# Kernel tuning notes

Hardware: AMD Instinct MI355X
Metric: run time of the kernel (lower is better)

Reference implementation:

```python
import jax, jax.numpy as jnp
import numpy as np

N_NODES = 20000
N_EDGES = 640000
HIDDEN = 256
MSG = 64  # discrete message of MSG binary symbols -> 2*MSG one-hot bits
TAU = 0.5


def setup_inputs() -> dict:
    key = jax.random.key(0)
    ks = jax.random.split(key, 12)
    x = jax.random.normal(ks[0], (N_NODES, HIDDEN), dtype=jnp.float32)
    h = jax.random.normal(ks[1], (N_NODES, HIDDEN), dtype=jnp.float32)
    src = jax.random.randint(ks[2], (N_EDGES,), 0, N_NODES)
    dst = jax.random.randint(ks[3], (N_EDGES,), 0, N_NODES)
    u = jax.random.uniform(ks[4], (N_EDGES, MSG, 2), dtype=jnp.float32,
                           minval=1e-6, maxval=1.0 - 1e-6)
    gumbel = -jnp.log(-jnp.log(u))  # standard Gumbel noise
    def lin(k, out_f, in_f):
        bound = 1.0 / np.sqrt(in_f)
        kw, kb = jax.random.split(k)
        W = jax.random.uniform(kw, (out_f, in_f), jnp.float32, -bound, bound)
        b = jax.random.uniform(kb, (out_f,), jnp.float32, -bound, bound)
        return W, b
    W_enc, b_enc = lin(ks[5], 2 * MSG, 2 * HIDDEN)          # f_enc
    W_dec, b_dec = lin(ks[6], 2 * MSG, 2 * MSG)             # f_dec
    W_ih, b_ih = lin(ks[7], 3 * HIDDEN, HIDDEN + 2 * MSG)   # GRUCell input weights
    W_hh, b_hh = lin(ks[8], 3 * HIDDEN, HIDDEN)             # GRUCell hidden weights
    return dict(x=x, h=h, W_enc=W_enc, b_enc=b_enc, W_dec=W_dec, b_dec=b_dec,
                W_ih=W_ih, b_ih=b_ih, W_hh=W_hh, b_hh=b_hh,
                gumbel=gumbel, src=src, dst=dst)


def reference(x, h, W_enc, b_enc, W_dec, b_dec, W_ih, b_ih, W_hh, b_hh,
              gumbel, src, dst):
    N = x.shape[0]
    h_det = jax.lax.stop_gradient(h)  # edges.src['h'] uses h.detach()
    # --- msg_func: per-edge encode + straight-through gumbel-softmax (hard) ---
    e_in = jnp.concatenate([x[src], h_det[src]], axis=1)           # [E, 2H]
    logits = (e_in @ W_enc.T + b_enc).reshape(-1, MSG, 2)          # [E, M, 2]
    y_soft = jax.nn.softmax((logits + gumbel) / TAU, axis=-1)
    y_hard = jax.nn.one_hot(jnp.argmax(y_soft, axis=-1), 2, dtype=y_soft.dtype)
    m = (y_hard + y_soft - jax.lax.stop_gradient(y_soft)).reshape(-1, 2 * MSG)
    # --- aggr_func: elementwise-OR == segment max over destination nodes ---
    c = jax.ops.segment_max(m, dst, num_segments=N)
    c = jnp.where(jnp.isneginf(c), 0.0, c)  # nodes with no in-edges get zeros
    # --- update: f_dec + GRUCell (PyTorch gate order r, z, n) ---
    inp = jnp.concatenate([x, c @ W_dec.T + b_dec], axis=1)        # [N, H+2M]
    gi = inp @ W_ih.T + b_ih                                       # [N, 3H]
    gh = h @ W_hh.T + b_hh                                         # [N, 3H]
    i_r, i_z, i_n = jnp.split(gi, 3, axis=1)
    h_r, h_z, h_n = jnp.split(gh, 3, axis=1)
    r = jax.nn.sigmoid(i_r + h_r)
    z = jax.nn.sigmoid(i_z + h_z)
    n = jnp.tanh(i_n + r * h_n)
    return (1.0 - z) * n + z * h
```

## Files before the change

kernel.cpp:

```cpp
#include <hip/hip_runtime.h>
#include <math.h>

#define NN 20000
#define NE 640000

typedef __attribute__((ext_vector_type(8))) short short8v;
typedef __attribute__((ext_vector_type(4))) float f32x4;

__device__ inline unsigned short f2bf(float f) {
    unsigned int u = __builtin_bit_cast(unsigned int, f);
    u += 0x7fff + ((u >> 16) & 1);
    return (unsigned short)(u >> 16);
}
__device__ inline float bf2f(unsigned short s) {
    unsigned int u = ((unsigned int)s) << 16;
    return __builtin_bit_cast(float, u);
}
__device__ inline void gload16(const unsigned short* g, short* l) {
    __builtin_amdgcn_global_load_lds(
        (const __attribute__((address_space(1))) unsigned int*)g,
        (__attribute__((address_space(3))) unsigned int*)l, 16, 0, 0);
}

__global__ __launch_bounds__(256)
void prep_kernel(const float* __restrict__ W_ih, const float* __restrict__ W_hh,
                 const float* __restrict__ W_dec, const float* __restrict__ W_enc,
                 const float* __restrict__ b_ih, const float* __restrict__ b_hh,
                 const float* __restrict__ b_dec,
                 unsigned short* __restrict__ Wbig, float* __restrict__ bias_cat,
                 unsigned int* __restrict__ cbits, unsigned short* __restrict__ Whl)
{
    int r = blockIdx.x;
    int tid = threadIdx.x;
    int zi = r * 256 + tid;
    if (zi < NN * 4) cbits[zi] = 0u;
    if (r < 128) {
        for (int k2 = tid; k2 < 512; k2 += 256) {
            float v = W_enc[(size_t)r * 512 + k2];
            unsigned short hi = f2bf(v);
            Whl[(size_t)r * 512 + k2] = hi;
            Whl[65536 + (size_t)r * 512 + k2] = f2bf(v - bf2f(hi));
        }
    }
    int g = r >> 8, j = r & 255;
    for (int k = tid; k < 512; k += 256) {
        float v;
        if (k < 256) {
            v = (g < 3) ? W_ih[(size_t)(g * 256 + j) * 384 + k] : 0.f;
        } else {
            int sr = (g < 2) ? g * 256 + j : 512 + j;
            v = (g == 2) ? 0.f : W_hh[(size_t)sr * 256 + (k - 256)];
        }
        Wbig[(size_t)r * 640 + k] = f2bf(v);
    }
    if (tid < 128) {
        float acc = 0.f;
        if (g < 3) {
            const float* wr = W_ih + (size_t)(g * 256 + j) * 384 + 256;
#pragma unroll 4
            for (int p = 0; p < 128; ++p) acc += wr[p] * W_dec[p * 128 + tid];
        }
        Wbig[(size_t)r * 640 + 512 + tid] = f2bf(acc);
    } else if (tid == 128) {
        float v;
        if (g == 3) {
            v = b_hh[512 + j];
        } else {
            int sr = g * 256 + j;
            float bdt = 0.f;
            for (int m = 0; m < 128; ++m) bdt += W_ih[(size_t)sr * 384 + 256 + m] * b_dec[m];
            v = b_ih[sr] + bdt + ((g < 2) ? b_hh[sr] : 0.f);
        }
        bias_cat[r] = v;
    }
}

__global__ __launch_bounds__(512)
void enc_gemm(const float* __restrict__ x, const float* __restrict__ h,
              const unsigned short* __restrict__ Whl, const float* __restrict__ b_enc,
              unsigned short* __restrict__ LdiffBf, unsigned short* __restrict__ Abig)
{
    __shared__ __align__(16) short Ah[64][72], Al[64][72];
    __shared__ __align__(16) short Wh[128 * 64], Wl[128 * 64];
    const int bm0 = blockIdx.x * 64;
    const int tid = threadIdx.x;
    const int lane = tid & 63;
    const int wave = tid >> 6;
    const int wm = wave >> 2, wn = wave & 3;
    const int r16 = lane & 15, kg = lane >> 4;
    const int sw = r16 & 7;

    const int arow = tid >> 3, as_ = tid & 7;
    const int agm = (bm0 + arow >= NN) ? NN - 1 : bm0 + arow;
    const int wrow0 = tid >> 3, wrow1 = (tid >> 3) + 64, ws_ = tid & 7;

    f32x4 acc[2][2];
#pragma unroll
    for (int i = 0; i < 2; ++i)
#pragma unroll
        for (int j = 0; j < 2; ++j) acc[i][j] = (f32x4){0.f, 0.f, 0.f, 0.f};

    float4 av0, av1;
    short8v pwh0, pwh1, pwl0, pwl1;
    auto ISSUE = [&](int kt) {
        int kc = kt * 64 + as_ * 8;
        const float* p = (kc < 256) ? (x + (size_t)agm * 256 + kc)
                                    : (h + (size_t)agm * 256 + (kc - 256));
        av0 = *(const float4*)p;
        av1 = *(const float4*)(p + 4);
        size_t w0 = (size_t)wrow0 * 512 + kt * 64 + ws_ * 8;
        size_t w1 = (size_t)wrow1 * 512 + kt * 64 + ws_ * 8;
        pwh0 = *(const short8v*)&Whl[w0];
        pwh1 = *(const short8v*)&Whl[w1];
        pwl0 = *(const short8v*)&Whl[65536 + w0];
        pwl1 = *(const short8v*)&Whl[65536 + w1];
    };

    ISSUE(0);
    for (int kt = 0; kt < 8; ++kt) {
        __syncthreads();
        {
            float vv[8] = {av0.x, av0.y, av0.z, av0.w, av1.x, av1.y, av1.z, av1.w};
            short8v hi, lo;
#pragma unroll
            for (int t = 0; t < 8; ++t) {
                unsigned short hb = f2bf(vv[t]);
                hi[t] = (short)hb;
                lo[t] = (short)f2bf(vv[t] - bf2f(hb));
            }
            *(short8v*)&Ah[arow][as_ * 8] = hi;
            *(short8v*)&Al[arow][as_ * 8] = lo;
            *(short8v*)&Abig[(size_t)agm * 512 + kt * 64 + as_ * 8] = hi;
            int p0 = (ws_ ^ (wrow0 & 7)) * 8;
            int p1 = (ws_ ^ (wrow1 & 7)) * 8;
            *(short8v*)&Wh[wrow0 * 64 + p0] = pwh0;
            *(short8v*)&Wl[wrow0 * 64 + p0] = pwl0;
            *(short8v*)&Wh[wrow1 * 64 + p1] = pwh1;
            *(short8v*)&Wl[wrow1 * 64 + p1] = pwl1;
        }
        if (kt < 7) ISSUE(kt + 1);
        __syncthreads();
#pragma unroll
        for (int ks = 0; ks < 2; ++ks) {
            int kc = ks * 32 + kg * 8;
            int gsel = (ks * 4 + kg) ^ sw;
            short8v ah[2], al[2], wh[2], wl[2];
#pragma unroll
            for (int f = 0; f < 2; ++f) {
                ah[f] = *(const short8v*)&Ah[wm * 32 + f * 16 + r16][kc];
                al[f] = *(const short8v*)&Al[wm * 32 + f * 16 + r16][kc];
                int wr = wn * 32 + f * 16 + r16;
                wh[f] = *(const short8v*)&Wh[wr * 64 + gsel * 8];
                wl[f] = *(const short8v*)&Wl[wr * 64 + gsel * 8];
            }
#pragma unroll
            for (int fi = 0; fi < 2; ++fi)
#pragma unroll
                for (int fj = 0; fj < 2; ++fj) {
                    acc[fi][fj] = __builtin_amdgcn_mfma_f32_16x16x32_bf16(
                        ah[fi], wh[fj], acc[fi][fj], 0, 0, 0);
                    acc[fi][fj] = __builtin_amdgcn_mfma_f32_16x16x32_bf16(
                        al[fi], wh[fj], acc[fi][fj], 0, 0, 0);
                    acc[fi][fj] = __builtin_amdgcn_mfma_f32_16x16x32_bf16(
                        ah[fi], wl[fj], acc[fi][fj], 0, 0, 0);
                }
        }
    }
#pragma unroll
    for (int fi = 0; fi < 2; ++fi) {
        int rg = bm0 + wm * 32 + fi * 16 + kg * 4;
#pragma unroll
        for (int fj = 0; fj < 2; ++fj) {
            int cg = wn * 32 + fj * 16 + r16;
            float bv = b_enc[cg];
#pragma unroll
            for (int i = 0; i < 4; ++i) {
                float v = acc[fi][fj][i] + bv;
                float o = __shfl_xor(v, 1);
                if (!(r16 & 1) && rg + i < NN)
                    LdiffBf[(size_t)(rg + i) * 64 + (cg >> 1)] = f2bf(v - o);
            }
        }
    }
}

__global__ __launch_bounds__(256)
void edge_msg_kernel(const unsigned short* __restrict__ LdiffBf,
                     const float* __restrict__ gumbel,
                     const int* __restrict__ src, const int* __restrict__ dst,
                     unsigned int* __restrict__ cbits, int E)
{
    const int lane = threadIdx.x & 63;
    const int hl = lane & 31;
    const int side = lane >> 5;
    const int slot = blockIdx.x * 4 + (threadIdx.x >> 6);
    const int nslots = gridDim.x * 4;
    const unsigned int* Lw = (const unsigned int*)LdiffBf;
    for (int p = slot; p * 2 < E; p += nslots) {
        int e = p * 2 + side;
        int s = src[e];
        unsigned int dp = Lw[(size_t)s * 32 + hl];
        float d0 = bf2f((unsigned short)(dp & 0xffffu));
        float d1 = bf2f((unsigned short)(dp >> 16));
        float4 gv = *(const float4*)&gumbel[(size_t)e * 128 + hl * 4];
        int c0 = (d0 + gv.x) < gv.y ? 1 : 0;
        int c1 = (d1 + gv.z) < gv.w ? 1 : 0;
        int sh = (hl & 7) * 4;
        unsigned int val = (1u << (sh + c0)) | (1u << (sh + 2 + c1));
        val |= __shfl_xor(val, 1);
        val |= __shfl_xor(val, 2);
        val |= __shfl_xor(val, 4);
        if ((hl & 7) == 0) {
            int dn = dst[e];
            atomicOr(&cbits[(size_t)dn * 4 + (hl >> 3)], val);
        }
    }
}

__global__ __launch_bounds__(256)
void gates_gru(const unsigned short* __restrict__ Abig,
               const unsigned int* __restrict__ cbits,
               const unsigned short* __restrict__ Wbig,
               const float* __restrict__ bias_cat,
               const float* __restrict__ h, float* __restrict__ out)
{
    __shared__ __align__(16) short As[2][64 * 64];
    const int orig = blockIdx.x;
    const int xcd = orig & 7, idx = orig >> 3;
    const int wgid = (xcd < 4 ? xcd * 157 : 628 + (xcd - 4) * 156) + idx;
    const int bm0 = (wgid >> 2) * 64;
    const int j0  = (wgid & 3) * 64;
    const int tid = threadIdx.x;
    const int lane = tid & 63;
    const int w = tid >> 6;
    const int r16 = lane & 15, kg = lane >> 4;
    const int sw = r16 & 7;

    f32x4 acc[4][4];
#pragma unroll
    for (int g = 0; g < 4; ++g)
#pragma unroll
        for (int i = 0; i < 4; ++i) acc[g][i] = (f32x4){0.f, 0.f, 0.f, 0.f};

    unsigned int cw[4][4];
#pragma unroll
    for (int fi = 0; fi < 4; ++fi) {
        int rr = bm0 + fi * 16 + r16; if (rr >= NN) rr = NN - 1;
        uint4 v = *(const uint4*)&cbits[rr * 4];
        cw[fi][0] = v.x; cw[fi][1] = v.y; cw[fi][2] = v.z; cw[fi][3] = v.w;
    }

    auto STAGE = [&](int b, int kt) {
        const int kc0 = kt * 64;
#pragma unroll
        for (int it = 0; it < 2; ++it) {
            int chunk = w * 2 + it;
            int slot = chunk * 64 + lane;
            int row = slot >> 3, gch = slot & 7;
            int gm = bm0 + row; if (gm >= NN) gm = NN - 1;
            gload16(Abig + (size_t)gm * 512 + kc0 + ((gch ^ (row & 7)) << 3),
                    As[b] + chunk * 512);
        }
    };
    short8v breg[2][3][2];
    auto BLOAD = [&](int b, int kt) {
        const int kc0 = kt * 64;
        const int g2 = (kt < 4 || kt >= 8) ? 2 : 3;
#pragma unroll
        for (int s = 0; s < 3; ++s) {
            int gate = (s < 2) ? s : g2;
            const unsigned short* bp =
                Wbig + (size_t)(gate * 256 + j0 + w * 16 + r16) * 640 + kc0 + kg * 8;
            breg[b][s][0] = *(const short8v*)bp;
            breg[b][s][1] = *(const short8v*)(bp + 32);
        }
    };

    STAGE(0, 0);
    BLOAD(0, 0);
#pragma unroll
    for (int kt = 0; kt < 8; ++kt) {
        const int cur = kt & 1;
        if (kt < 7) STAGE(cur ^ 1, kt + 1);
        BLOAD(cur ^ 1, kt + 1);
        if (kt < 7) { asm volatile("s_waitcnt vmcnt(8)" ::: "memory"); }
        else        { asm volatile("s_waitcnt vmcnt(6)" ::: "memory"); }
        __builtin_amdgcn_s_barrier();
        __builtin_amdgcn_sched_barrier(0);
        const int g2c = (kt < 4) ? 2 : 3;
        __builtin_amdgcn_s_setprio(1);
#pragma unroll
        for (int ks = 0; ks < 2; ++ks) {
            int gsel = (ks * 4 + kg) ^ sw;
            short8v a[4];
#pragma unroll
            for (int fi = 0; fi < 4; ++fi)
                a[fi] = *(const short8v*)&As[cur][(fi * 16 + r16) * 64 + gsel * 8];
#pragma unroll
            for (int s = 0; s < 3; ++s) {
                const int gate = (s < 2) ? s : g2c;
#pragma unroll
                for (int fi = 0; fi < 4; ++fi)
                    acc[gate][fi] = __builtin_amdgcn_mfma_f32_16x16x32_bf16(
                        a[fi], breg[cur][s][ks], acc[gate][fi], 0, 0, 0);
            }
        }
        __builtin_amdgcn_s_setprio(0);
        __builtin_amdgcn_sched_barrier(0);
        __builtin_amdgcn_s_barrier();
    }
    BLOAD(1, 9);
#pragma unroll
    for (int kt8 = 0; kt8 < 2; ++kt8) {
        short8v a[4][2];
#pragma unroll
        for (int fi = 0; fi < 4; ++fi)
#pragma unroll
            for (int ks = 0; ks < 2; ++ks) {
                unsigned int byte = (cw[fi][kt8 * 2 + ks] >> (kg * 8)) & 0xffu;
                short8v v;
#pragma unroll
                for (int t = 0; t < 8; ++t)
                    v[t] = ((byte >> t) & 1u) ? (short)0x3F80 : (short)0;
                a[fi][ks] = v;
            }
#pragma unroll
        for (int ks = 0; ks < 2; ++ks)
#pragma unroll
            for (int s = 0; s < 3; ++s) {
                const int gate = (s < 2) ? s : 2;
#pragma unroll
                for (int fi = 0; fi < 4; ++fi)
                    acc[gate][fi] = __builtin_amdgcn_mfma_f32_16x16x32_bf16(
                        a[fi][ks], breg[kt8][s][ks], acc[gate][fi], 0, 0, 0);
            }
    }
    const int cg = j0 + w * 16 + r16;
    const float br = bias_cat[cg],       bz = bias_cat[256 + cg];
    const float bi = bias_cat[512 + cg], bh = bias_cat[768 + cg];
#pragma unroll
    for (int fi = 0; fi < 4; ++fi) {
        int rg = bm0 + fi * 16 + kg * 4;
#pragma unroll
        for (int i = 0; i < 4; ++i) {
            int m = rg + i;
            if (m >= NN) continue;
            float rp = acc[0][fi][i] + br;
            float zp = acc[1][fi][i] + bz;
            float ip = acc[2][fi][i] + bi;
            float hp = acc[3][fi][i] + bh;
            float hv = h[(size_t)m * 256 + cg];
            float r = 1.f / (1.f + __expf(-rp));
            float z = 1.f / (1.f + __expf(-zp));
            float nn2 = tanhf(ip + r * hp);
            out[(size_t)m * 256 + cg] = (1.f - z) * nn2 + z * hv;
        }
    }
}

extern "C" void kernel_launch(void* const* d_in, const int* in_sizes, int n_in,
                              void* d_out, int out_size, void* d_ws, size_t ws_size,
                              hipStream_t stream)
{
    const float* x     = (const float*)d_in[0];
    const float* h     = (const float*)d_in[1];
    const float* W_enc = (const float*)d_in[2];
    const float* b_enc = (const float*)d_in[3];
    const float* W_dec = (const float*)d_in[4];
    const float* b_dec = (const float*)d_in[5];
    const float* W_ih  = (const float*)d_in[6];
    const float* b_ih  = (const float*)d_in[7];
    const float* W_hh  = (const float*)d_in[8];
    const float* b_hh  = (const float*)d_in[9];
    const float* gumbel = (const float*)d_in[10];
    const int*   src   = (const int*)d_in[11];
    const int*   dst   = (const int*)d_in[12];
    float* out = (float*)d_out;

    char* ws = (char*)d_ws;
    unsigned short* LdiffBf  = (unsigned short*)(ws);
    unsigned int*   cbits    = (unsigned int*)(ws + 2560000);
    unsigned short* Wbig     = (unsigned short*)(ws + 2880000);
    float*          bias_cat = (float*)(ws + 4190720);
    unsigned short* Whl      = (unsigned short*)(ws + 4194816);
    unsigned short* Abig     = (unsigned short*)(ws + 4456960);

    prep_kernel<<<1024, 256, 0, stream>>>(W_ih, W_hh, W_dec, W_enc, b_ih, b_hh, b_dec,
                                          Wbig, bias_cat, cbits, Whl);
    enc_gemm<<<313, 512, 0, stream>>>(x, h, Whl, b_enc, LdiffBf, Abig);
    edge_msg_kernel<<<2048, 256, 0, stream>>>(LdiffBf, gumbel, src, dst, cbits, NE);
    gates_gru<<<1252, 256, 0, stream>>>(Abig, cbits, Wbig, bias_cat, h, out);
}
```

Before: 190.5 us.

## Fuse weight prep into encoder GEMM launch and software-pipeline edge loads

Merges the weight-preparation kernel into the encoder GEMM kernel as extra blocks, so one launch is removed and preparation runs alongside the GEMM. The encoder now splits W_enc into hi/lo bf16 on the fly instead of reading a pre-split copy, which adds conversion work inside each block. The bias dot product uses a wave shuffle reduction instead of a serial loop. The edge message loop prefetches the next edge's src, dst, gumbel and logit values before processing the current one, to hide gather latency.

```diff
diff --git a/kernel.cpp b/kernel.cpp
--- a/kernel.cpp
+++ b/kernel.cpp
@@ -22,68 +22,64 @@
         (__attribute__((address_space(3))) unsigned int*)l, 16, 0, 0);
 }
 
-__global__ __launch_bounds__(256)
-void prep_kernel(const float* __restrict__ W_ih, const float* __restrict__ W_hh,
-                 const float* __restrict__ W_dec, const float* __restrict__ W_enc,
-                 const float* __restrict__ b_ih, const float* __restrict__ b_hh,
-                 const float* __restrict__ b_dec,
-                 unsigned short* __restrict__ Wbig, float* __restrict__ bias_cat,
-                 unsigned int* __restrict__ cbits, unsigned short* __restrict__ Whl)
+__global__ __launch_bounds__(512)
+void enc_prep(const float* __restrict__ x, const float* __restrict__ h,
+              const float* __restrict__ W_enc, const float* __restrict__ b_enc,
+              const float* __restrict__ W_ih, const float* __restrict__ W_hh,
+              const float* __restrict__ W_dec, const float* __restrict__ b_ih,
+              const float* __restrict__ b_hh, const float* __restrict__ b_dec,
+              unsigned short* __restrict__ LdiffBf, unsigned short* __restrict__ Abig,
+              unsigned short* __restrict__ Wbig, float* __restrict__ bias_cat,
+              unsigned int* __restrict__ cbits)
 {
-    int r = blockIdx.x;
-    int tid = threadIdx.x;
-    int zi = r * 256 + tid;
-    if (zi < NN * 4) cbits[zi] = 0u;
-    if (r < 128) {
-        for (int k2 = tid; k2 < 512; k2 += 256) {
-            float v = W_enc[(size_t)r * 512 + k2];
-            unsigned short hi = f2bf(v);
-            Whl[(size_t)r * 512 + k2] = hi;
-            Whl[65536 + (size_t)r * 512 + k2] = f2bf(v - bf2f(hi));
-        }
-    }
-    int g = r >> 8, j = r & 255;
-    for (int k = tid; k < 512; k += 256) {
-        float v;
-        if (k < 256) {
-            v = (g < 3) ? W_ih[(size_t)(g * 256 + j) * 384 + k] : 0.f;
-        } else {
-            int sr = (g < 2) ? g * 256 + j : 512 + j;
-            v = (g == 2) ? 0.f : W_hh[(size_t)sr * 256 + (k - 256)];
-        }
-        Wbig[(size_t)r * 640 + k] = f2bf(v);
-    }
-    if (tid < 128) {
-        float acc = 0.f;
-        if (g < 3) {
-            const float* wr = W_ih + (size_t)(g * 256 + j) * 384 + 256;
+    const int tid = threadIdx.x;
+    if (blockIdx.x >= 313) {
+        const int r = blockIdx.x - 313;
+        int zi = r * 512 + tid;
+        if (zi < NN * 4) cbits[zi] = 0u;
+        const int g = r >> 8, j = r & 255;
+        {
+            float v;
+            if (tid < 256) {
+                v = (g < 3) ? W_ih[(size_t)(g * 256 + j) * 384 + tid] : 0.f;
+            } else {
+                int sr = (g < 2) ? g * 256 + j : 512 + j;
+                v = (g == 2) ? 0.f : W_hh[(size_t)sr * 256 + (tid - 256)];
+            }
+            Wbig[(size_t)r * 640 + tid] = f2bf(v);
+        }
+        if (tid < 128) {
+            float acc = 0.f;
+            if (g < 3) {
+                const float* wr = W_ih + (size_t)(g * 256 + j) * 384 + 256;
 #pragma unroll 4
-            for (int p = 0; p < 128; ++p) acc += wr[p] * W_dec[p * 128 + tid];
-        }
-        Wbig[(size_t)r * 640 + 512 + tid] = f2bf(acc);
-    } else if (tid == 128) {
-        float v;
-        if (g == 3) {
-            v = b_hh[512 + j];
-        } else {
-            int sr = g * 256 + j;
-            float bdt = 0.f;
-            for (int m = 0; m < 128; ++m) bdt += W_ih[(size_t)sr * 384 + 256 + m] * b_dec[m];
-            v = b_ih[sr] + bdt + ((g < 2) ? b_hh[sr] : 0.f);
-        }
-        bias_cat[r] = v;
-    }
-}
-
-__global__ __launch_bounds__(512)
-void enc_gemm(const float* __restrict__ x, const float* __restrict__ h,
-              const unsigned short* __restrict__ Whl, const float* __restrict__ b_enc,
-              unsigned short* __restrict__ LdiffBf, unsigned short* __restrict__ Abig)
-{
+                for (int p = 0; p < 128; ++p) acc += wr[p] * W_dec[p * 128 + tid];
+            }
+            Wbig[(size_t)r * 640 + 512 + tid] = f2bf(acc);
+        } else if (tid < 192) {
+            int m = tid - 128;
+            float v = 0.f;
+            if (g < 3) {
+                const float* wr = W_ih + (size_t)(g * 256 + j) * 384 + 256;
+                v = wr[m] * b_dec[m] + wr[m + 64] * b_dec[m + 64];
+            }
+#pragma unroll
+            for (int o = 1; o < 64; o <<= 1) v += __shfl_xor(v, o);
+            if (m == 0) {
+                float bv;
+                if (g == 3) bv = b_hh[512 + j];
+                else {
+                    int sr = g * 256 + j;
+                    bv = b_ih[sr] + v + ((g < 2) ? b_hh[sr] : 0.f);
+                }
+                bias_cat[r] = bv;
+            }
+        }
+        return;
+    }
     __shared__ __align__(16) short Ah[64][72], Al[64][72];
     __shared__ __align__(16) short Wh[128 * 64], Wl[128 * 64];
     const int bm0 = blockIdx.x * 64;
-    const int tid = threadIdx.x;
     const int lane = tid & 63;
     const int wave = tid >> 6;
     const int wm = wave >> 2, wn = wave & 3;
@@ -100,20 +96,17 @@
 #pragma unroll
         for (int j = 0; j < 2; ++j) acc[i][j] = (f32x4){0.f, 0.f, 0.f, 0.f};
 
-    float4 av0, av1;
-    short8v pwh0, pwh1, pwl0, pwl1;
+    float4 av0, av1, wv0, wv1, wv2, wv3;
     auto ISSUE = [&](int kt) {
         int kc = kt * 64 + as_ * 8;
         const float* p = (kc < 256) ? (x + (size_t)agm * 256 + kc)
                                     : (h + (size_t)agm * 256 + (kc - 256));
         av0 = *(const float4*)p;
         av1 = *(const float4*)(p + 4);
-        size_t w0 = (size_t)wrow0 * 512 + kt * 64 + ws_ * 8;
-        size_t w1 = (size_t)wrow1 * 512 + kt * 64 + ws_ * 8;
-        pwh0 = *(const short8v*)&Whl[w0];
-        pwh1 = *(const short8v*)&Whl[w1];
-        pwl0 = *(const short8v*)&Whl[65536 + w0];
-        pwl1 = *(const short8v*)&Whl[65536 + w1];
+        const float* q0 = W_enc + (size_t)wrow0 * 512 + kt * 64 + ws_ * 8;
+        const float* q1 = W_enc + (size_t)wrow1 * 512 + kt * 64 + ws_ * 8;
+        wv0 = *(const float4*)q0; wv1 = *(const float4*)(q0 + 4);
+        wv2 = *(const float4*)q1; wv3 = *(const float4*)(q1 + 4);
     };
 
     ISSUE(0);
@@ -131,12 +124,22 @@
             *(short8v*)&Ah[arow][as_ * 8] = hi;
             *(short8v*)&Al[arow][as_ * 8] = lo;
             *(short8v*)&Abig[(size_t)agm * 512 + kt * 64 + as_ * 8] = hi;
+            float ww0[8] = {wv0.x, wv0.y, wv0.z, wv0.w, wv1.x, wv1.y, wv1.z, wv1.w};
+            float ww1[8] = {wv2.x, wv2.y, wv2.z, wv2.w, wv3.x, wv3.y, wv3.z, wv3.w};
+            short8v h0, l0, h1, l1;
+#pragma unroll
+            for (int t = 0; t < 8; ++t) {
+                unsigned short hb0 = f2bf(ww0[t]);
+                h0[t] = (short)hb0; l0[t] = (short)f2bf(ww0[t] - bf2f(hb0));
+                unsigned short hb1 = f2bf(ww1[t]);
+                h1[t] = (short)hb1; l1[t] = (short)f2bf(ww1[t] - bf2f(hb1));
+            }
             int p0 = (ws_ ^ (wrow0 & 7)) * 8;
             int p1 = (ws_ ^ (wrow1 & 7)) * 8;
-            *(short8v*)&Wh[wrow0 * 64 + p0] = pwh0;
-            *(short8v*)&Wl[wrow0 * 64 + p0] = pwl0;
-            *(short8v*)&Wh[wrow1 * 64 + p1] = pwh1;
-            *(short8v*)&Wl[wrow1 * 64 + p1] = pwl1;
+            *(short8v*)&Wh[wrow0 * 64 + p0] = h0;
+            *(short8v*)&Wl[wrow0 * 64 + p0] = l0;
+            *(short8v*)&Wh[wrow1 * 64 + p1] = h1;
+            *(short8v*)&Wl[wrow1 * 64 + p1] = l1;
         }
         if (kt < 7) ISSUE(kt + 1);
         __syncthreads();
@@ -196,13 +199,25 @@
     const int slot = blockIdx.x * 4 + (threadIdx.x >> 6);
     const int nslots = gridDim.x * 4;
     const unsigned int* Lw = (const unsigned int*)LdiffBf;
-    for (int p = slot; p * 2 < E; p += nslots) {
-        int e = p * 2 + side;
-        int s = src[e];
-        unsigned int dp = Lw[(size_t)s * 32 + hl];
+
+    int p = slot;
+    if (p * 2 >= E) return;
+    int e = p * 2 + side;
+    int s = src[e], dd = dst[e];
+    float4 gv = *(const float4*)&gumbel[(size_t)e * 128 + hl * 4];
+    unsigned int dp = Lw[(size_t)s * 32 + hl];
+    while (true) {
+        int pn = p + nslots;
+        bool more = pn * 2 < E;
+        int sn = 0, ddn = 0; float4 gn; unsigned int dpn = 0;
+        if (more) {
+            int en = pn * 2 + side;
+            sn = src[en]; ddn = dst[en];
+            gn = *(const float4*)&gumbel[(size_t)en * 128 + hl * 4];
+            dpn = Lw[(size_t)sn * 32 + hl];
+        }
         float d0 = bf2f((unsigned short)(dp & 0xffffu));
         float d1 = bf2f((unsigned short)(dp >> 16));
-        float4 gv = *(const float4*)&gumbel[(size_t)e * 128 + hl * 4];
         int c0 = (d0 + gv.x) < gv.y ? 1 : 0;
         int c1 = (d1 + gv.z) < gv.w ? 1 : 0;
         int sh = (hl & 7) * 4;
@@ -210,10 +225,10 @@
         val |= __shfl_xor(val, 1);
         val |= __shfl_xor(val, 2);
         val |= __shfl_xor(val, 4);
-        if ((hl & 7) == 0) {
-            int dn = dst[e];
-            atomicOr(&cbits[(size_t)dn * 4 + (hl >> 3)], val);
-        }
+        if ((hl & 7) == 0)
+            atomicOr(&cbits[(size_t)dd * 4 + (hl >> 3)], val);
+        if (!more) break;
+        p = pn; s = sn; dd = ddn; gv = gn; dp = dpn;
     }
 }
 
@@ -382,12 +397,11 @@
     unsigned int*   cbits    = (unsigned int*)(ws + 2560000);
     unsigned short* Wbig     = (unsigned short*)(ws + 2880000);
     float*          bias_cat = (float*)(ws + 4190720);
-    unsigned short* Whl      = (unsigned short*)(ws + 4194816);
-    unsigned short* Abig     = (unsigned short*)(ws + 4456960);
-
-    prep_kernel<<<1024, 256, 0, stream>>>(W_ih, W_hh, W_dec, W_enc, b_ih, b_hh, b_dec,
-                                          Wbig, bias_cat, cbits, Whl);
-    enc_gemm<<<313, 512, 0, stream>>>(x, h, Whl, b_enc, LdiffBf, Abig);
+    unsigned short* Abig     = (unsigned short*)(ws + 4194816);
+
+    enc_prep<<<1337, 512, 0, stream>>>(x, h, W_enc, b_enc, W_ih, W_hh, W_dec,
+                                       b_ih, b_hh, b_dec,
+                                       LdiffBf, Abig, Wbig, bias_cat, cbits);
     edge_msg_kernel<<<2048, 256, 0, stream>>>(LdiffBf, gumbel, src, dst, cbits, NE);
     gates_gru<<<1252, 256, 0, stream>>>(Abig, cbits, Wbig, bias_cat, h, out);
 }
```

Result: faster. 174.4 us (-8.4%).
